# Kernel tuning notes

Measured on AMD Instinct MI355X. Metric: run time of the kernel, lower is better.

The kernel has to match this reference:

```python
import jax, jax.numpy as jnp
import numpy as np

B, T, C, HS, WS = 16, 16, 128, 32, 32

def _conv1x1(w, b, t):
    # w: [Cout, Cin], t: [B, Cin, H, W] -> [B, Cout, H, W]
    return jnp.einsum('oi,bihw->bohw', w, t) + b[None, :, None, None]

def setup_inputs() -> dict:
    key = jax.random.key(0)
    ks = jax.random.split(key, 6)
    x = jax.random.normal(ks[0], (B, T, C, HS, WS), dtype=jnp.float32)
    c0 = jax.random.normal(ks[1], (B, C, HS, WS), dtype=jnp.float32) * 1e-6
    # conv1..conv5: Cin=C; conv6..conv13: Cin=2C
    W5 = jax.random.normal(ks[2], (5, C, C), dtype=jnp.float32) * 0.05
    b5 = jax.random.normal(ks[3], (5, C), dtype=jnp.float32) * 0.05
    W8 = jax.random.normal(ks[4], (8, C, 2 * C), dtype=jnp.float32) * 0.05
    b8 = jax.random.normal(ks[5], (8, C), dtype=jnp.float32) * 0.05
    return {"x": x, "c0": c0, "W5": W5, "b5": b5, "W8": W8, "b8": b8}

def _self_attention_memory(W5, b5, W8, b8, m, h):
    vh = _conv1x1(W5[0], b5[0], h)            # conv1
    kh = _conv1x1(W5[1], b5[1], h)            # conv2
    qh = _conv1x1(W5[2], b5[2], h)            # conv3
    qh = jnp.swapaxes(qh, 2, 3)               # transpose spatial (needs H==W)
    ah = jax.nn.softmax(kh * qh, axis=-1)
    zh = vh * ah
    km = _conv1x1(W5[3], b5[3], m)            # conv4
    vm = _conv1x1(W5[4], b5[4], m)            # conv5
    am = jax.nn.softmax(qh * km, axis=-1)
    zm = vm * am
    z = _conv1x1(W8[0], b8[0], jnp.concatenate((zh, zm), axis=1))  # conv6
    hz = jnp.concatenate((h, z), axis=1)
    ot = jax.nn.sigmoid(_conv1x1(W8[1], b8[1], hz))   # conv7
    gt = jnp.tanh(_conv1x1(W8[2], b8[2], hz))         # conv8
    it = jax.nn.sigmoid(_conv1x1(W8[3], b8[3], hz))   # conv9
    mt = gt * it + (1.0 - it) * m
    ht = ot * mt
    return mt, ht

def _forward(x, c0, W5, b5, W8, b8):
    xt = jnp.transpose(x, (1, 0, 2, 3, 4))   # [T, B, C, H, W]
    mem0 = jnp.zeros_like(xt[0])
    h0 = jnp.zeros_like(xt[0])

    def step(carry, xi):
        mem, H, Cst = carry
        hx = jnp.concatenate((H, xi), axis=1)
        a_xh = jax.nn.sigmoid(_conv1x1(W8[4], b8[4], hx))   # conv10
        ga = jax.nn.sigmoid(_conv1x1(W8[5], b8[5], hx))     # conv11
        gv = jnp.tanh(_conv1x1(W8[6], b8[6], hx))           # conv12
        Cst = Cst * a_xh + ga * gv
        a_xh1 = jax.nn.sigmoid(_conv1x1(W8[7], b8[7], hx))  # conv13
        H = a_xh1 * jnp.tanh(Cst)
        mem, H = _self_attention_memory(W5, b5, W8, b8, mem, H)
        return (mem, H, Cst), None

    (mem, H, Cst), _ = jax.lax.scan(step, (mem0, h0, c0), xt)
    return H

def reference(x, c0, W5, b5, W8, b8):
    return _forward(x, c0, W5, b5, W8, b8)
```

## Files before the change

kernel.cpp:

```cpp
#include <hip/hip_runtime.h>
#include <hip/hip_bf16.h>

#define BB 16
#define TT 16
#define CC 128
#define HW 1024
#define PIX (CC*HW)
#define STOT ((long)BB*PIX)

#define TW16 4096
#define WI16 131072
#define WZ16 262144
#define XW16 2097152

typedef short short8 __attribute__((ext_vector_type(8)));
typedef float f32x4  __attribute__((ext_vector_type(4)));

__device__ __forceinline__ float sigf(float x) { return 1.0f / (1.0f + __expf(-x)); }
__device__ __forceinline__ float tanhf_fast(float x) {
    float ax = fabsf(x);
    float t = __expf(-2.0f * ax);
    float r = (1.0f - t) / (1.0f + t);
    return copysignf(r, x);
}

__device__ __forceinline__ unsigned short pack_bf16(float x) {
    unsigned u = __float_as_uint(x);
    return (unsigned short)((u + 0x7fffu + ((u >> 16) & 1u)) >> 16);
}
__device__ __forceinline__ float bf16f(unsigned short s) {
    return __uint_as_float(((unsigned)s) << 16);
}

__device__ __forceinline__ long bidx16(int p, int c, int nkt) {
    int kb = (c >> 3) & 3;
    int phys = ((p & 127) + (kb << 4)) & 127;
    return ((long)((p >> 7) * nkt + (c >> 5)) << 12) + (kb << 10) + (phys << 3) + (c & 7);
}

typedef __attribute__((address_space(3))) unsigned lds_u32_t;
typedef __attribute__((address_space(1))) const unsigned gbl_u32_t;
__device__ __forceinline__ void gld16(const void* g, unsigned* l) {
    __builtin_amdgcn_global_load_lds((gbl_u32_t*)g, (lds_u32_t*)l, 16, 0, 0);
}

template<int MODE>
__global__ __launch_bounds__(256, 2) void gemm_mfma(
    const unsigned short* __restrict__ Wp, const float* __restrict__ bias,
    const unsigned short* __restrict__ imgA, long wA,
    const unsigned short* __restrict__ imgB, long wB, int nktB,
    int k_split, int m_split,
    void* __restrict__ outv, void* __restrict__ stv,
    unsigned short* __restrict__ simg, float* __restrict__ Hout,
    int M, int K)
{
    __shared__ __align__(16) unsigned As[2048];
    __shared__ __align__(16) unsigned Bs[2048];

    const int b  = blockIdx.z;
    const int n0 = blockIdx.x * 128;
    const int m0 = blockIdx.y * 128;
    const int t  = threadIdx.x;
    const int lane = t & 63;
    const int w  = t >> 6;
    const int wm = w & 1, wn = w >> 1;
    const int g  = lane >> 4, pl = lane & 15;

    f32x4 acc[4][4] = {};

    for (int k0 = 0; k0 < K; k0 += 32) {
        {
            const char* gA = (const char*)(Wp +
                (size_t)((m0 >> 7) * (K >> 5) + (k0 >> 5)) * TW16);
            gld16(gA + t * 16, As + t * 4);
            gld16(gA + 4096 + t * 16, As + 1024 + t * 4);
        }
        const bool useB = (m0 >= m_split) || (k0 >= k_split);
        {
            const int kc = useB ? (k0 - ((m0 >= m_split) ? 0 : k_split)) : k0;
            const unsigned short* img = useB ? imgB : imgA;
            const long bw = useB ? wB : wA;
            const int nkt = useB ? nktB : 4;
            const char* gB = (const char*)(img + (long)b * bw +
                ((long)((n0 >> 7) * nkt + (kc >> 5)) << 12));
            gld16(gB + t * 16, Bs + t * 4);
            gld16(gB + 4096 + t * 16, Bs + 1024 + t * 4);
        }
        __syncthreads();

        short8 afr[4], bfr[4];
        #pragma unroll
        for (int mt = 0; mt < 4; ++mt) {
            int row = 64 * wm + 16 * mt + pl;
            int phys = (row + (g << 4)) & 127;
            afr[mt] = *(const short8*)((const char*)As + g * 2048 + phys * 16);
        }
        #pragma unroll
        for (int nt = 0; nt < 4; ++nt) {
            int prow = 64 * wn + 16 * nt + pl;
            int phys = (prow + (g << 4)) & 127;
            bfr[nt] = *(const short8*)((const char*)Bs + g * 2048 + phys * 16);
        }
        #pragma unroll
        for (int mt = 0; mt < 4; ++mt)
            #pragma unroll
            for (int nt = 0; nt < 4; ++nt)
                acc[mt][nt] = __builtin_amdgcn_mfma_f32_16x16x32_bf16(afr[mt], bfr[nt], acc[mt][nt], 0, 0, 0);
        __syncthreads();
    }

    if (MODE == 1) {
        #pragma unroll
        for (int mt = 0; mt < 4; ++mt)
            #pragma unroll
            for (int r = 0; r < 4; ++r) {
                int row = m0 + 64 * wm + 16 * mt + 4 * g + r;
                float bb = bias[row];
                #pragma unroll
                for (int nt = 0; nt < 4; ++nt) {
                    int col = n0 + 64 * wn + 16 * nt + pl;
                    ((unsigned short*)outv)[((long)b * M + row) * HW + col] =
                        pack_bf16(acc[mt][nt][r] + bb);
                }
            }
    } else {
        const float4* bias4 = (const float4*)bias;
        unsigned short* Hp = (unsigned short*)outv;
        #pragma unroll
        for (int mt = 0; mt < 4; ++mt) {
            int c = (m0 >> 2) + 16 * wm + 4 * mt + g;
            float4 bb = bias4[c];
            #pragma unroll
            for (int nt = 0; nt < 4; ++nt) {
                int p = n0 + 64 * wn + 16 * nt + pl;
                long lidx = (long)b * PIX + (long)c * HW + p;
                long widx = (long)b * WI16 + bidx16(p, c, 4);
                float v0 = acc[mt][nt][0] + bb.x;
                float v1 = acc[mt][nt][1] + bb.y;
                float v2 = acc[mt][nt][2] + bb.z;
                float v3 = acc[mt][nt][3] + bb.w;
                if (MODE == 2) {
                    float* Cst = (float*)stv;
                    float cc = Cst[lidx] * sigf(v0) + sigf(v1) * tanhf_fast(v2);
                    Cst[lidx] = cc;
                    Hp[widx] = pack_bf16(sigf(v3) * tanhf_fast(cc));
                } else {
                    float* mpf = (float*)stv;
                    float ot = sigf(v0), gt = tanhf_fast(v1), it = sigf(v2);
                    float mo = mpf[lidx];
                    float mn = gt * it + (1.0f - it) * mo;
                    mpf[lidx] = mn;
                    simg[widx] = pack_bf16(mn);
                    float hv = ot * mn;
                    Hp[widx] = pack_bf16(hv);
                    if (Hout) Hout[lidx] = hv;
                }
            }
        }
    }
}

__global__ __launch_bounds__(1024) void attn_kernel(
    const unsigned short* __restrict__ VKM, unsigned short* __restrict__ Zimg)
{
    __shared__ float qs[4][32 * 33];
    const int tid = threadIdx.x;
    const int b = blockIdx.x >> 5, cq = blockIdx.x & 31;
    const int c0 = cq << 2;
    const long base = (long)b * 640 * HW;

    #pragma unroll
    for (int cc = 0; cc < 4; ++cc)
        qs[cc][(tid >> 5) * 33 + (tid & 31)] =
            bf16f(VKM[base + (long)(256 + c0 + cc) * HW + tid]);
    __syncthreads();

    const int i = tid >> 5, j = tid & 31;
    unsigned short zh[4], zm[4];
    #pragma unroll
    for (int cc = 0; cc < 4; ++cc) {
        const long cbs = base + (long)(c0 + cc) * HW;
        float qhT = qs[cc][j * 33 + i];
        float vh  = bf16f(VKM[cbs + tid]);
        float kh  = bf16f(VKM[cbs + 128l * HW + tid]);
        float km  = bf16f(VKM[cbs + 384l * HW + tid]);
        float vm  = bf16f(VKM[cbs + 512l * HW + tid]);

        float sh = kh * qhT, sm = qhT * km;
        float mh = sh, mm = sm;
        #pragma unroll
        for (int o = 16; o > 0; o >>= 1) {
            mh = fmaxf(mh, __shfl_xor(mh, o, 32));
            mm = fmaxf(mm, __shfl_xor(mm, o, 32));
        }
        float eh = __expf(sh - mh), em = __expf(sm - mm);
        float s1 = eh, s2 = em;
        #pragma unroll
        for (int o = 16; o > 0; o >>= 1) {
            s1 += __shfl_xor(s1, o, 32);
            s2 += __shfl_xor(s2, o, 32);
        }
        zh[cc] = pack_bf16(vh * (eh / s1));
        zm[cc] = pack_bf16(vm * (em / s2));
    }
    const int kt = c0 >> 5, kb = (c0 >> 3) & 3, sl = c0 & 7;
    const int phys = ((tid & 127) + (kb << 4)) & 127;
    long e16 = (long)b * WZ16 + ((long)((tid >> 7) * 8 + kt) << 12) +
               (kb << 10) + (phys << 3) + sl;
    uint2 oh, om;
    oh.x = (unsigned)zh[0] | ((unsigned)zh[1] << 16);
    oh.y = (unsigned)zh[2] | ((unsigned)zh[3] << 16);
    om.x = (unsigned)zm[0] | ((unsigned)zm[1] << 16);
    om.y = (unsigned)zm[2] | ((unsigned)zm[3] << 16);
    *(uint2*)(Zimg + e16)              = oh;
    *(uint2*)(Zimg + e16 + (4l << 12)) = om;
}

__global__ __launch_bounds__(256) void pack_x(
    const float* __restrict__ x, uint4* __restrict__ Xp, int tstart, int oneshot)
{
    long q = (long)blockIdx.x * 256 + threadIdx.x;
    long e = q << 3;
    int t = tstart + (int)(e >> 21);
    long r = e & ((1l << 21) - 1);
    int b = (int)(r >> 17);
    int v = (int)(r & ((1 << 17) - 1));
    int tile = v >> 12;
    int pt = tile >> 2, kt = tile & 3;
    int ww = v & 4095;
    int kb = ww >> 10, phys = (ww >> 3) & 127;
    int row = (phys - (kb << 4)) & 127;
    int p = (pt << 7) + row;
    int c = (kt << 5) + (kb << 3);
    const float* xs = x + (((long)b * TT + t) * CC + c) * HW + p;
    union { unsigned short s[8]; uint4 u; } o;
    #pragma unroll
    for (int jj = 0; jj < 8; ++jj)
        o.s[jj] = pack_bf16(xs[(long)jj * HW]);
    Xp[oneshot ? q : (q & ((1l << 18) - 1))] = o.u;
}

__device__ __forceinline__ void wimg(unsigned short* img, int Ktiles, int r, int k, float v) {
    int tile = (r >> 7) * Ktiles + (k >> 5);
    int row = r & 127, ks = k & 31;
    int kb = ks >> 3;
    int phys = (row + (kb << 4)) & 127;
    img[(size_t)tile * TW16 + (kb << 10) + (phys << 3) + (ks & 7)] = pack_bf16(v);
}

__global__ __launch_bounds__(256) void setup_all(
    const float* __restrict__ W5, const float* __restrict__ W8, const float* __restrict__ b8,
    unsigned short* __restrict__ Wp5i,
    unsigned short* __restrict__ Wgi, float* __restrict__ bg4,
    unsigned short* __restrict__ Woi, float* __restrict__ bo4)
{
    int idx = blockIdx.x * 256 + threadIdx.x;
    if (idx < 81920) {
        int r = idx >> 7, k = idx & 127;
        wimg(Wp5i, 4, r, k, W5[idx]);
        return;
    }
    idx -= 81920;
    if (idx < 131072) {
        int rr = idx >> 8, k = idx & 255;
        int c = rr >> 2, gg = rr & 3;
        wimg(Wgi, 8, rr, k, W8[((long)(4 + gg) * 128 + c) * 256 + k]);
        if (k == 0) bg4[rr] = b8[(4 + gg) * 128 + c];
        return;
    }
    idx -= 131072;
    if (idx >= 512 * 384) return;
    int rr = idx / 384, k = idx - rr * 384;
    int c = rr >> 2, gg = rr & 3;
    float wv = 0.0f;
    if (gg < 3) {
        const float* wr = W8 + ((long)(1 + gg) * 128 + c) * 256;
        if (k < 128) {
            wv = wr[k];
        } else {
            int i = k - 128;
            float s = 0.0f;
            for (int j = 0; j < 128; ++j)
                s += wr[128 + j] * W8[(long)j * 256 + i];
            wv = s;
        }
    }
    wimg(Woi, 12, rr, k, wv);
    if (k == 0) {
        float bb = 0.0f;
        if (gg < 3) {
            bb = b8[(1 + gg) * 128 + c];
            const float* wr = W8 + ((long)(1 + gg) * 128 + c) * 256;
            for (int j = 0; j < 128; ++j) bb += wr[128 + j] * b8[j];
        }
        bo4[rr] = bb;
    }
}

extern "C" void kernel_launch(void* const* d_in, const int* in_sizes, int n_in,
                              void* d_out, int out_size, void* d_ws, size_t ws_size,
                              hipStream_t stream)
{
    const float* x  = (const float*)d_in[0];
    const float* c0 = (const float*)d_in[1];
    const float* W5 = (const float*)d_in[2];
    const float* b5 = (const float*)d_in[3];
    const float* W8 = (const float*)d_in[4];
    const float* b8 = (const float*)d_in[5];
    float* out = (float*)d_out;

    const long S = STOT;
    unsigned short* Ha  = (unsigned short*)d_ws;
    unsigned short* Hb  = Ha + 16l * WI16;
    unsigned short* mpi = Hb + 16l * WI16;
    float* mpf = (float*)(mpi + 16l * WI16);
    float* Cst = mpf + S;
    unsigned short* Wp5i = (unsigned short*)(Cst + S);
    unsigned short* Wgi  = Wp5i + 20 * TW16;
    unsigned short* Woi  = Wgi + 32 * TW16;
    float* bg4 = (float*)(Woi + 48 * TW16);
    float* bo4 = bg4 + 512;
    unsigned short* VKM  = (unsigned short*)(bo4 + 512);
    unsigned short* Zimg = VKM + 5 * S;
    unsigned short* Xp   = Zimg + 16l * WZ16;

    const bool havex =
        ((char*)(Xp + 16l * XW16) - (char*)d_ws) <= (long)ws_size;

    hipMemsetAsync(Hb,  0, 16l * WI16 * 2, stream);
    hipMemsetAsync(mpi, 0, 16l * WI16 * 2, stream);
    hipMemsetAsync(mpf, 0, S * sizeof(float), stream);
    hipMemcpyAsync(Cst, c0, S * sizeof(float), hipMemcpyDeviceToDevice, stream);

    setup_all<<<1600, dim3(256), 0, stream>>>(W5, W8, b8, Wp5i, Wgi, bg4, Woi, bo4);
    if (havex)
        pack_x<<<16384, dim3(256), 0, stream>>>(x, (uint4*)Xp, 0, 1);

    const int BIG = 1 << 30;
    const dim3 blk(256);
    for (int t = 0; t < TT; ++t) {
        if (!havex)
            pack_x<<<1024, dim3(256), 0, stream>>>(x, (uint4*)Xp, t, 0);
        const unsigned short* Xpt = Xp + (havex ? (long)t * XW16 : 0l);

        gemm_mfma<2><<<dim3(8, 4, 16), blk, 0, stream>>>(
            Wgi, bg4, Hb, (long)WI16, Xpt, (long)WI16, 4,
            128, BIG, Ha, Cst, nullptr, nullptr, 512, 256);

        gemm_mfma<1><<<dim3(8, 5, 16), blk, 0, stream>>>(
            Wp5i, b5, Ha, (long)WI16, mpi, (long)WI16, 4,
            BIG, 384, VKM, nullptr, nullptr, nullptr, 640, 128);

        attn_kernel<<<512, dim3(1024), 0, stream>>>(VKM, Zimg);

        gemm_mfma<3><<<dim3(8, 4, 16), blk, 0, stream>>>(
            Woi, bo4, Ha, (long)WI16, Zimg, (long)WZ16, 8,
            128, BIG, Hb, mpf, mpi, (t == TT - 1) ? out : nullptr, 512, 384);
    }
}
```

Baseline: 1.122 ms.

## Double-buffer LDS tiles and widen K step to 64 in MFMA GEMM

The GEMM kernel now keeps two LDS buffers for A and B, each holding a 64-wide K chunk. The next chunk is prefetched with global_load_lds while MFMAs run on the current one, and there is one barrier per iteration instead of two. The goal is to hide global-load latency and halve the number of synchronisations. LDS use per block grows from 16KB to 64KB, which could limit the two-blocks-per-CU occupancy. There also appears to be no wait for the async loads to land before the barrier, which is a correctness risk.

```diff
diff --git a/kernel.cpp b/kernel.cpp
--- a/kernel.cpp
+++ b/kernel.cpp
@@ -54,8 +54,8 @@
     unsigned short* __restrict__ simg, float* __restrict__ Hout,
     int M, int K)
 {
-    __shared__ __align__(16) unsigned As[2048];
-    __shared__ __align__(16) unsigned Bs[2048];
+    __shared__ __align__(16) unsigned As[2][4096];
+    __shared__ __align__(16) unsigned Bs[2][4096];
 
     const int b  = blockIdx.z;
     const int n0 = blockIdx.x * 128;
@@ -65,48 +65,62 @@
     const int w  = t >> 6;
     const int wm = w & 1, wn = w >> 1;
     const int g  = lane >> 4, pl = lane & 15;
+    const int nk64 = K >> 6;
 
     f32x4 acc[4][4] = {};
 
-    for (int k0 = 0; k0 < K; k0 += 32) {
-        {
-            const char* gA = (const char*)(Wp +
-                (size_t)((m0 >> 7) * (K >> 5) + (k0 >> 5)) * TW16);
-            gld16(gA + t * 16, As + t * 4);
-            gld16(gA + 4096 + t * 16, As + 1024 + t * 4);
-        }
-        const bool useB = (m0 >= m_split) || (k0 >= k_split);
-        {
-            const int kc = useB ? (k0 - ((m0 >= m_split) ? 0 : k_split)) : k0;
-            const unsigned short* img = useB ? imgB : imgA;
-            const long bw = useB ? wB : wA;
-            const int nkt = useB ? nktB : 4;
-            const char* gB = (const char*)(img + (long)b * bw +
-                ((long)((n0 >> 7) * nkt + (kc >> 5)) << 12));
-            gld16(gB + t * 16, Bs + t * 4);
-            gld16(gB + 4096 + t * 16, Bs + 1024 + t * 4);
-        }
+    auto stageA = [&](int kchunk, unsigned* dst) {
+        const char* gA = (const char*)(Wp +
+            (size_t)((m0 >> 7) * (K >> 5) + (kchunk >> 5)) * TW16);
+        gld16(gA + t * 16, dst + t * 4);
+        gld16(gA + 4096 + t * 16, dst + 1024 + t * 4);
+    };
+    auto stageB = [&](int kchunk, unsigned* dst) {
+        const bool useB = (m0 >= m_split) || (kchunk >= k_split);
+        const int kc = useB ? (kchunk - ((m0 >= m_split) ? 0 : k_split)) : kchunk;
+        const unsigned short* img = useB ? imgB : imgA;
+        const long bw = useB ? wB : wA;
+        const int nkt = useB ? nktB : 4;
+        const char* gB = (const char*)(img + (long)b * bw +
+            ((long)((n0 >> 7) * nkt + (kc >> 5)) << 12));
+        gld16(gB + t * 16, dst + t * 4);
+        gld16(gB + 4096 + t * 16, dst + 1024 + t * 4);
+    };
+    auto stage = [&](int k0, int buf) {
+        stageA(k0,      As[buf]);
+        stageA(k0 + 32, As[buf] + 2048);
+        stageB(k0,      Bs[buf]);
+        stageB(k0 + 32, Bs[buf] + 2048);
+    };
+
+    stage(0, 0);
+
+    for (int it = 0; it < nk64; ++it) {
+        const int buf = it & 1;
         __syncthreads();
-
-        short8 afr[4], bfr[4];
-        #pragma unroll
-        for (int mt = 0; mt < 4; ++mt) {
-            int row = 64 * wm + 16 * mt + pl;
-            int phys = (row + (g << 4)) & 127;
-            afr[mt] = *(const short8*)((const char*)As + g * 2048 + phys * 16);
-        }
-        #pragma unroll
-        for (int nt = 0; nt < 4; ++nt) {
-            int prow = 64 * wn + 16 * nt + pl;
-            int phys = (prow + (g << 4)) & 127;
-            bfr[nt] = *(const short8*)((const char*)Bs + g * 2048 + phys * 16);
-        }
-        #pragma unroll
-        for (int mt = 0; mt < 4; ++mt)
-            #pragma unroll
-            for (int nt = 0; nt < 4; ++nt)
-                acc[mt][nt] = __builtin_amdgcn_mfma_f32_16x16x32_bf16(afr[mt], bfr[nt], acc[mt][nt], 0, 0, 0);
-        __syncthreads();
+        if (it + 1 < nk64) stage((it + 1) << 6, buf ^ 1);
+
+        #pragma unroll
+        for (int h = 0; h < 2; ++h) {
+            short8 afr[4], bfr[4];
+            #pragma unroll
+            for (int mt = 0; mt < 4; ++mt) {
+                int row = 64 * wm + 16 * mt + pl;
+                int phys = (row + (g << 4)) & 127;
+                afr[mt] = *(const short8*)((const char*)As[buf] + h * 8192 + g * 2048 + phys * 16);
+            }
+            #pragma unroll
+            for (int nt = 0; nt < 4; ++nt) {
+                int prow = 64 * wn + 16 * nt + pl;
+                int phys = (prow + (g << 4)) & 127;
+                bfr[nt] = *(const short8*)((const char*)Bs[buf] + h * 8192 + g * 2048 + phys * 16);
+            }
+            #pragma unroll
+            for (int mt = 0; mt < 4; ++mt)
+                #pragma unroll
+                for (int nt = 0; nt < 4; ++nt)
+                    acc[mt][nt] = __builtin_amdgcn_mfma_f32_16x16x32_bf16(afr[mt], bfr[nt], acc[mt][nt], 0, 0, 0);
+        }
     }
 
     if (MODE == 1) {
@@ -146,9 +160,9 @@
                     Hp[widx] = pack_bf16(sigf(v3) * tanhf_fast(cc));
                 } else {
                     float* mpf = (float*)stv;
-                    float ot = sigf(v0), gt = tanhf_fast(v1), it = sigf(v2);
+                    float ot = sigf(v0), gt = tanhf_fast(v1), it2 = sigf(v2);
                     float mo = mpf[lidx];
-                    float mn = gt * it + (1.0f - it) * mo;
+                    float mn = gt * it2 + (1.0f - it2) * mo;
                     mpf[lidx] = mn;
                     simg[widx] = pack_bf16(mn);
                     float hv = ot * mn;
```

New measurement: 1.085 ms. 3.3% less time.
